# Optimization experiments

Measured on AMD Instinct MI355X. Metric: run time of the kernel, lower is better.

The kernel has to match this reference:

```python
import jax, jax.numpy as jnp
import numpy as np

N_NODES = 40000
N_EDGES = 640000
N_GRAPHS = 64
DIM_IN = 32
N_EDGE_TYPE = 16
DH = 128
DOUT = 256
T = 4


def setup_inputs() -> dict:
    key = jax.random.key(0)
    ks = jax.random.split(key, 16)
    inp = {
        "x": jax.random.normal(ks[0], (N_NODES, DIM_IN), dtype=jnp.float32),
        "edge_index": jax.random.randint(ks[1], (2, N_EDGES), 0, N_NODES, dtype=jnp.int64),
        "edge_attr": jax.random.normal(ks[2], (N_EDGES, N_EDGE_TYPE), dtype=jnp.float32),
        "graph_ids": jnp.sort(jax.random.randint(ks[3], (N_NODES,), 0, N_GRAPHS, dtype=jnp.int64)),
    }
    s = lambda fan_in: 1.0 / np.sqrt(fan_in)
    inp["Wn"] = jax.random.uniform(ks[4], (DIM_IN, DH), jnp.float32, -s(DIM_IN), s(DIM_IN))
    inp["bn"] = jnp.zeros((DH,), jnp.float32)
    inp["We"] = jax.random.uniform(ks[5], (N_EDGE_TYPE, DH), jnp.float32, -s(N_EDGE_TYPE), s(N_EDGE_TYPE))
    inp["be"] = jnp.zeros((DH,), jnp.float32)
    inp["W1"] = jax.random.uniform(ks[6], (DH, DH), jnp.float32, -s(DH), s(DH))
    inp["b1"] = jnp.zeros((DH,), jnp.float32)
    inp["W2"] = jax.random.uniform(ks[7], (DH, DH), jnp.float32, -s(DH), s(DH))
    inp["b2"] = jnp.zeros((DH,), jnp.float32)
    inp["Wl"] = jax.random.uniform(ks[8], (DH * T, DOUT), jnp.float32, -s(DH * T), s(DH * T))
    inp["bl"] = jnp.zeros((DOUT,), jnp.float32)
    return inp


def reference(x, edge_index, edge_attr, graph_ids, Wn, bn, We, be, W1, b1, W2, b2, Wl, bl):
    # node / edge input transforms
    h = x @ Wn + bn                      # [N, DH]
    e = edge_attr @ We + be              # [E, DH]
    src, dst = edge_index[0], edge_index[1]

    def mlp(z):
        return jax.nn.relu(z @ W1 + b1) @ W2 + b2

    all_h = []
    for _ in range(T):
        # GINE: message = relu(x_src + edge_attr), scatter-sum to dst
        msg = jax.nn.relu(h[src] + e)                                 # [E, DH]
        agg = jax.ops.segment_sum(msg, dst, num_segments=N_NODES)     # [N, DH]
        h = mlp(h + agg)                                              # eps = 0 -> (1+eps)*x = x
        all_h.append(h)

    all_x = jnp.concatenate(all_h, axis=-1)                           # [N, DH*T]
    pooled = jax.ops.segment_sum(all_x, graph_ids, num_segments=N_GRAPHS)  # [G, DH*T]
    return pooled @ Wl + bl                                           # [G, DOUT]
```

## Files before the change

kernel.cpp:

```cpp
#include <hip/hip_runtime.h>

#define N_NODES   40000
#define N_EDGES   640000
#define N_GRAPHS  64
#define DIM_IN    32
#define N_ETYPE   16
#define DH        128
#define DOUT      256
#define T_ITERS   4
#define SCAN_BLK  40

typedef unsigned int uint32;
typedef unsigned short ushort16;
typedef __attribute__((ext_vector_type(8))) short bf16x8;
typedef __attribute__((ext_vector_type(4))) float f32x4;

__device__ __forceinline__ uint32 f2bf1(float f) {
  uint32 u = __float_as_uint(f);
  return (u + 0x7fffu + ((u >> 16) & 1u)) >> 16;
}
__device__ __forceinline__ uint32 pack_bf2(float lo, float hi) {
  return (f2bf1(hi) << 16) | f2bf1(lo);
}

__global__ __launch_bounds__(256) void k_embed(const float* __restrict__ x,
                                               const float* __restrict__ Wn,
                                               const float* __restrict__ bn,
                                               float* __restrict__ h,
                                               ushort16* __restrict__ hb) {
  int idx = blockIdx.x * 256 + threadIdx.x;
  int n = idx >> 7, c = idx & 127;
  const float* xr = x + n * DIM_IN;
  float acc = bn[c];
#pragma unroll
  for (int k = 0; k < DIM_IN; ++k)
    acc = fmaf(xr[k], Wn[k * DH + c], acc);
  h[idx] = acc;
  hb[idx] = (ushort16)f2bf1(acc);
}

__global__ __launch_bounds__(256) void k_hist(const int* __restrict__ dst,
                                              int* __restrict__ counts) {
  int i = blockIdx.x * 256 + threadIdx.x;
  atomicAdd(&counts[dst[i]], 1);
}

__global__ __launch_bounds__(1024) void k_scan1(const int* __restrict__ counts,
                                                int* __restrict__ excl,
                                                int* __restrict__ blk_sums) {
  __shared__ int wsums[16];
  int tid = threadIdx.x, lane = tid & 63, w = tid >> 6;
  int i = blockIdx.x * 1024 + tid;
  int v = (i < N_NODES) ? counts[i] : 0;
  int s = v;
#pragma unroll
  for (int off = 1; off < 64; off <<= 1) {
    int t = __shfl_up(s, off);
    if (lane >= off) s += t;
  }
  if (lane == 63) wsums[w] = s;
  __syncthreads();
  if (tid < 16) {
    int ws_ = wsums[tid];
#pragma unroll
    for (int off = 1; off < 16; off <<= 1) {
      int t = __shfl_up(ws_, off);
      if (tid >= off) ws_ += t;
    }
    wsums[tid] = ws_;
  }
  __syncthreads();
  int e = s - v + (w ? wsums[w - 1] : 0);
  if (i < N_NODES) excl[i] = e;
  if (tid == 0) blk_sums[blockIdx.x] = wsums[15];
}

__global__ __launch_bounds__(64) void k_scan2(const int* __restrict__ blk_sums,
                                              int* __restrict__ blk_off,
                                              int* __restrict__ row_start) {
  int lane = threadIdx.x;
  int v = (lane < SCAN_BLK) ? blk_sums[lane] : 0;
  int s = v;
#pragma unroll
  for (int off = 1; off < 64; off <<= 1) {
    int t = __shfl_up(s, off);
    if (lane >= off) s += t;
  }
  if (lane < SCAN_BLK) blk_off[lane] = s - v;
  if (lane == 63) row_start[N_NODES] = s;
}

__global__ __launch_bounds__(1024) void k_scan3(int* __restrict__ row_start,
                                                const int* __restrict__ blk_off,
                                                int* __restrict__ cursor) {
  int i = blockIdx.x * 1024 + threadIdx.x;
  if (i < N_NODES) {
    int v = row_start[i] + blk_off[blockIdx.x];
    row_start[i] = v;
    cursor[i] = v;
  }
}

__global__ __launch_bounds__(256) void k_permute(const int* __restrict__ src,
                                                 const int* __restrict__ dst,
                                                 int* __restrict__ cursor,
                                                 int* __restrict__ src_perm,
                                                 int* __restrict__ eid_perm) {
  int i = blockIdx.x * 256 + threadIdx.x;
  int d = dst[i];
  int pos = atomicAdd(&cursor[d], 1);
  src_perm[pos] = src[i];
  eid_perm[pos] = i;
}

__global__ __launch_bounds__(256) void k_permute_ea(const int* __restrict__ src,
                                                    const int* __restrict__ dst,
                                                    const float4* __restrict__ edge_attr,
                                                    int* __restrict__ cursor,
                                                    int* __restrict__ src_perm,
                                                    float4* __restrict__ ea_perm) {
  int i = blockIdx.x * 256 + threadIdx.x;
  int d = dst[i];
  int pos = atomicAdd(&cursor[d], 1);
  src_perm[pos] = src[i];
  const float4* s = edge_attr + ((size_t)i << 2);
  float4* o = ea_perm + ((size_t)pos << 2);
  float4 v0 = s[0], v1 = s[1], v2 = s[2], v3 = s[3];
  o[0] = v0; o[1] = v1; o[2] = v2; o[3] = v3;
}

#define MAC16(A0,A1,A2,A3)                                          \
  p0 = fmaf(A0.x, we0[0], p0);  p1 = fmaf(A0.x, we1[0], p1);        \
  p0 = fmaf(A0.y, we0[1], p0);  p1 = fmaf(A0.y, we1[1], p1);        \
  p0 = fmaf(A0.z, we0[2], p0);  p1 = fmaf(A0.z, we1[2], p1);        \
  p0 = fmaf(A0.w, we0[3], p0);  p1 = fmaf(A0.w, we1[3], p1);        \
  p0 = fmaf(A1.x, we0[4], p0);  p1 = fmaf(A1.x, we1[4], p1);        \
  p0 = fmaf(A1.y, we0[5], p0);  p1 = fmaf(A1.y, we1[5], p1);        \
  p0 = fmaf(A1.z, we0[6], p0);  p1 = fmaf(A1.z, we1[6], p1);        \
  p0 = fmaf(A1.w, we0[7], p0);  p1 = fmaf(A1.w, we1[7], p1);        \
  p0 = fmaf(A2.x, we0[8], p0);  p1 = fmaf(A2.x, we1[8], p1);        \
  p0 = fmaf(A2.y, we0[9], p0);  p1 = fmaf(A2.y, we1[9], p1);        \
  p0 = fmaf(A2.z, we0[10], p0); p1 = fmaf(A2.z, we1[10], p1);       \
  p0 = fmaf(A2.w, we0[11], p0); p1 = fmaf(A2.w, we1[11], p1);       \
  p0 = fmaf(A3.x, we0[12], p0); p1 = fmaf(A3.x, we1[12], p1);       \
  p0 = fmaf(A3.y, we0[13], p0); p1 = fmaf(A3.y, we1[13], p1);       \
  p0 = fmaf(A3.z, we0[14], p0); p1 = fmaf(A3.z, we1[14], p1);       \
  p0 = fmaf(A3.w, we0[15], p0); p1 = fmaf(A3.w, we1[15], p1);

#define RELU_ACC(G)                                                  \
  acc0 += fmaxf(__uint_as_float((G) << 16) + p0, 0.0f);              \
  acc1 += fmaxf(__uint_as_float((G) & 0xffff0000u) + p1, 0.0f);

#define ACC2(G,E)                                                                 \
  acc0 += fmaxf(__uint_as_float((G) << 16) + __uint_as_float((E) << 16), 0.0f);   \
  acc1 += fmaxf(__uint_as_float((G) & 0xffff0000u) +                              \
                __uint_as_float((E) & 0xffff0000u), 0.0f);

__global__ __launch_bounds__(256) void k_perm_e(const int* __restrict__ src,
                                                const int* __restrict__ dst,
                                                const float4* __restrict__ edge_attr,
                                                const float* __restrict__ We,
                                                const float* __restrict__ be,
                                                int* __restrict__ cursor,
                                                int* __restrict__ src_perm,
                                                uint32* __restrict__ e_perm) {
  __shared__ float4 sAttr[1024];
  __shared__ int spos[256];
  int tid = threadIdx.x;
  int i = blockIdx.x * 256 + tid;
  int d = dst[i];
  int pos = atomicAdd(&cursor[d], 1);
  src_perm[pos] = src[i];
  spos[tid] = pos;
  size_t blockBase = (size_t)blockIdx.x * 1024;
  for (int idx = tid; idx < 1024; idx += 256)
    sAttr[idx] = edge_attr[blockBase + idx];
  __syncthreads();
  int lane = tid & 63, wv = tid >> 6;
  int c = lane << 1;
  float we0[N_ETYPE], we1[N_ETYPE];
#pragma unroll
  for (int k = 0; k < N_ETYPE; ++k) {
    we0[k] = We[k * DH + c];
    we1[k] = We[k * DH + c + 1];
  }
  float be0 = be[c], be1 = be[c + 1];
  const float4* a = &sAttr[wv << 8];
  const int* wp = &spos[wv << 6];
#pragma unroll 2
  for (int j = 0; j < 64; ++j) {
    int pos_j = wp[j];
    float4 a0 = a[j * 4 + 0], a1 = a[j * 4 + 1], a2 = a[j * 4 + 2], a3 = a[j * 4 + 3];
    float p0 = be0, p1 = be1;
    MAC16(a0, a1, a2, a3)
    e_perm[((size_t)pos_j << 6) + lane] = pack_bf2(p0, p1);
  }
}

__global__ __launch_bounds__(256) void k_agg_lite(const float* __restrict__ h,
                                                  const uint32* __restrict__ hb,
                                                  const uint32* __restrict__ e_perm,
                                                  const int* __restrict__ row_start,
                                                  const int* __restrict__ src_perm,
                                                  uint32* __restrict__ zb) {
  int lane = threadIdx.x & 63;
  int n = (blockIdx.x << 2) + (threadIdx.x >> 6);
  int c = lane << 1;
  float2 hself = *(const float2*)&h[(size_t)n * DH + c];
  float acc0 = hself.x, acc1 = hself.y;
  int beg = row_start[n], end = row_start[n + 1];
  const uint32* ep = e_perm + ((size_t)beg << 6) + lane;
  const int* sp = src_perm + beg;
  int m = end - beg;
  int i = 0;
  for (; i + 16 <= m; i += 16, ep += 1024, sp += 16) {
    int ss[16];
    uint32 gg[16], ee[16];
#pragma unroll
    for (int k = 0; k < 16; ++k) ss[k] = sp[k];
#pragma unroll
    for (int k = 0; k < 16; ++k) gg[k] = hb[((size_t)ss[k] << 6) + lane];
#pragma unroll
    for (int k = 0; k < 16; ++k) ee[k] = ep[k * 64];
#pragma unroll
    for (int k = 0; k < 16; ++k) { ACC2(gg[k], ee[k]) }
  }
  for (; i + 4 <= m; i += 4, ep += 256, sp += 4) {
    int ss[4];
    uint32 gg[4], ee[4];
#pragma unroll
    for (int k = 0; k < 4; ++k) ss[k] = sp[k];
#pragma unroll
    for (int k = 0; k < 4; ++k) gg[k] = hb[((size_t)ss[k] << 6) + lane];
#pragma unroll
    for (int k = 0; k < 4; ++k) ee[k] = ep[k * 64];
#pragma unroll
    for (int k = 0; k < 4; ++k) { ACC2(gg[k], ee[k]) }
  }
  for (; i < m; ++i, ep += 64, ++sp) {
    int s0 = sp[0];
    uint32 g0 = hb[((size_t)s0 << 6) + lane];
    uint32 e0 = ep[0];
    ACC2(g0, e0)
  }
  zb[(size_t)n * 64 + lane] = pack_bf2(acc0, acc1);
}

__global__ __launch_bounds__(256) void k_agg_seq(const float* __restrict__ h,
                                                 const uint32* __restrict__ hb,
                                                 const float4* __restrict__ ea_perm,
                                                 const float* __restrict__ We,
                                                 const float* __restrict__ be,
                                                 const int* __restrict__ row_start,
                                                 const int* __restrict__ src_perm,
                                                 float* __restrict__ z) {
  int lane = threadIdx.x & 63;
  int n = (blockIdx.x << 2) + (threadIdx.x >> 6);
  int c = lane << 1;
  float we0[N_ETYPE], we1[N_ETYPE];
#pragma unroll
  for (int k = 0; k < N_ETYPE; ++k) {
    we0[k] = We[k * DH + c];
    we1[k] = We[k * DH + c + 1];
  }
  float be0 = be[c], be1 = be[c + 1];
  float2 hself = *(const float2*)&h[(size_t)n * DH + c];
  float acc0 = hself.x, acc1 = hself.y;
  int beg = row_start[n], end = row_start[n + 1];
  const float4* ea = ea_perm + ((size_t)beg << 2);
  int i = beg;
  for (; i + 4 <= end; i += 4, ea += 16) {
    int s0 = src_perm[i], s1 = src_perm[i + 1], s2 = src_perm[i + 2], s3 = src_perm[i + 3];
    uint32 g0 = hb[((size_t)s0 << 6) + lane];
    uint32 g1 = hb[((size_t)s1 << 6) + lane];
    uint32 g2 = hb[((size_t)s2 << 6) + lane];
    uint32 g3 = hb[((size_t)s3 << 6) + lane];
    float4 a0 = ea[0], a1 = ea[1], a2 = ea[2], a3 = ea[3];
    float4 b0 = ea[4], b1v = ea[5], b2v = ea[6], b3 = ea[7];
    float p0, p1;
    p0 = be0; p1 = be1; MAC16(a0, a1, a2, a3) RELU_ACC(g0)
    p0 = be0; p1 = be1; MAC16(b0, b1v, b2v, b3) RELU_ACC(g1)
    a0 = ea[8]; a1 = ea[9]; a2 = ea[10]; a3 = ea[11];
    b0 = ea[12]; b1v = ea[13]; b2v = ea[14]; b3 = ea[15];
    p0 = be0; p1 = be1; MAC16(a0, a1, a2, a3) RELU_ACC(g2)
    p0 = be0; p1 = be1; MAC16(b0, b1v, b2v, b3) RELU_ACC(g3)
  }
  for (; i < end; ++i, ea += 4) {
    int s0 = src_perm[i];
    uint32 g0 = hb[((size_t)s0 << 6) + lane];
    float4 a0 = ea[0], a1 = ea[1], a2 = ea[2], a3 = ea[3];
    float p0 = be0, p1 = be1;
    MAC16(a0, a1, a2, a3) RELU_ACC(g0)
  }
  *(float2*)&z[(size_t)n * DH + c] = make_float2(acc0, acc1);
}

__global__ __launch_bounds__(256, 8) void k_agg_ind(const float* __restrict__ h,
                                                    const uint32* __restrict__ hb,
                                                    const float* __restrict__ edge_attr,
                                                    const float* __restrict__ We,
                                                    const float* __restrict__ be,
                                                    const int* __restrict__ row_start,
                                                    const int* __restrict__ src_perm,
                                                    const int* __restrict__ eid_perm,
                                                    float* __restrict__ z) {
  int lane = threadIdx.x & 63;
  int n = (blockIdx.x << 2) + (threadIdx.x >> 6);
  int c = lane << 1;
  float we0[N_ETYPE], we1[N_ETYPE];
#pragma unroll
  for (int k = 0; k < N_ETYPE; ++k) {
    we0[k] = We[k * DH + c];
    we1[k] = We[k * DH + c + 1];
  }
  float be0 = be[c], be1 = be[c + 1];
  float2 hself = *(const float2*)&h[(size_t)n * DH + c];
  float acc0 = hself.x, acc1 = hself.y;
  int beg = row_start[n], end = row_start[n + 1];
  int i = beg;
  for (; i + 1 < end; i += 2) {
    int s0 = src_perm[i], s1 = src_perm[i + 1];
    int e0i = eid_perm[i], e1i = eid_perm[i + 1];
    uint32 g0 = hb[((size_t)s0 << 6) + lane];
    uint32 g1 = hb[((size_t)s1 << 6) + lane];
    const float4* eA = (const float4*)(edge_attr + (size_t)e0i * N_ETYPE);
    const float4* eB = (const float4*)(edge_attr + (size_t)e1i * N_ETYPE);
    float4 a0 = eA[0], a1 = eA[1], a2 = eA[2], a3 = eA[3];
    float p0, p1;
    p0 = be0; p1 = be1; MAC16(a0, a1, a2, a3) RELU_ACC(g0)
    float4 b0 = eB[0], b1v = eB[1], b2v = eB[2], b3 = eB[3];
    p0 = be0; p1 = be1; MAC16(b0, b1v, b2v, b3) RELU_ACC(g1)
  }
  if (i < end) {
    int s0 = src_perm[i];
    int e0i = eid_perm[i];
    uint32 g0 = hb[((size_t)s0 << 6) + lane];
    const float4* eA = (const float4*)(edge_attr + (size_t)e0i * N_ETYPE);
    float4 a0 = eA[0], a1 = eA[1], a2 = eA[2], a3 = eA[3];
    float p0 = be0, p1 = be1;
    MAC16(a0, a1, a2, a3) RELU_ACC(g0)
  }
  *(float2*)&z[(size_t)n * DH + c] = make_float2(acc0, acc1);
}

__global__ __launch_bounds__(256) void k_prep_w(const float* __restrict__ W1,
                                                const float* __restrict__ W2,
                                                ushort16* __restrict__ w1t,
                                                ushort16* __restrict__ w2t) {
  int id = blockIdx.x * 256 + threadIdx.x;
  int which = id >> 14;
  int rem = id & 16383;
  int k = rem >> 7, n = rem & 127;
  const float* W = which ? W2 : W1;
  ushort16* wt = which ? w2t : w1t;
  wt[n * 128 + k] = (ushort16)f2bf1(W[k * 128 + n]);
}

__global__ __launch_bounds__(256) void k_mlp_mfma(const uint32* __restrict__ zb,
                                                  const ushort16* __restrict__ w1t,
                                                  const ushort16* __restrict__ w2t,
                                                  const float* __restrict__ b1,
                                                  const float* __restrict__ b2,
                                                  const int* __restrict__ graph_ids,
                                                  float* __restrict__ h_out,
                                                  ushort16* __restrict__ hb_out,
                                                  float* __restrict__ pooled,
                                                  int t_slot) {
  __shared__ ushort16 sW[128 * 136];
  __shared__ ushort16 sA[64 * 136];
  int tid = threadIdx.x;
  int rb = blockIdx.x * 64;

  for (int idx = tid; idx < 1024; idx += 256) {
    int row = idx >> 4, ch = idx & 15;
    *(uint4*)&sA[row * 136 + ch * 8] = *(const uint4*)&zb[(size_t)(rb + row) * 64 + ch * 4];
  }
  for (int idx = tid; idx < 2048; idx += 256) {
    int row = idx >> 4, ch = idx & 15;
    *(uint4*)&sW[row * 136 + ch * 8] = *(const uint4*)&w1t[row * 128 + ch * 8];
  }
  __syncthreads();

  int l = tid & 63, w = tid >> 6;
  int r = l & 15, g = l >> 4;

  f32x4 acc[8];
#pragma unroll
  for (int n = 0; n < 8; ++n) {
    float bv = b1[n * 16 + r];
    acc[n] = (f32x4){bv, bv, bv, bv};
  }
#pragma unroll
  for (int k0 = 0; k0 < 4; ++k0) {
    bf16x8 a = *(const bf16x8*)&sA[(w * 16 + r) * 136 + k0 * 32 + g * 8];
#pragma unroll
    for (int n = 0; n < 8; ++n) {
      bf16x8 b = *(const bf16x8*)&sW[(n * 16 + r) * 136 + k0 * 32 + g * 8];
      acc[n] = __builtin_amdgcn_mfma_f32_16x16x32_bf16(a, b, acc[n], 0, 0, 0);
    }
  }
#pragma unroll
  for (int n = 0; n < 8; ++n) {
#pragma unroll
    for (int q = 0; q < 4; ++q) {
      float v = fmaxf(acc[n][q], 0.0f);
      sA[(w * 16 + g * 4 + q) * 136 + n * 16 + r] = (ushort16)f2bf1(v);
    }
  }
  __syncthreads();
  for (int idx = tid; idx < 2048; idx += 256) {
    int row = idx >> 4, ch = idx & 15;
    *(uint4*)&sW[row * 136 + ch * 8] = *(const uint4*)&w2t[row * 128 + ch * 8];
  }
  __syncthreads();

#pragma unroll
  for (int n = 0; n < 8; ++n) {
    float bv = b2[n * 16 + r];
    acc[n] = (f32x4){bv, bv, bv, bv};
  }
#pragma unroll
  for (int k0 = 0; k0 < 4; ++k0) {
    bf16x8 a = *(const bf16x8*)&sA[(w * 16 + r) * 136 + k0 * 32 + g * 8];
#pragma unroll
    for (int n = 0; n < 8; ++n) {
      bf16x8 b = *(const bf16x8*)&sW[(n * 16 + r) * 136 + k0 * 32 + g * 8];
      acc[n] = __builtin_amdgcn_mfma_f32_16x16x32_bf16(a, b, acc[n], 0, 0, 0);
    }
  }

  int node0 = rb + w * 16;
#pragma unroll
  for (int n = 0; n < 8; ++n) {
#pragma unroll
    for (int q = 0; q < 4; ++q) {
      int node = node0 + g * 4 + q;
      float v = acc[n][q];
      h_out[(size_t)node * DH + n * 16 + r] = v;
      hb_out[(size_t)node * DH + n * 16 + r] = (ushort16)f2bf1(v);
    }
  }
  float* pbase = pooled + t_slot * DH;
  int gid0 = graph_ids[node0];
  if (gid0 == graph_ids[node0 + 15]) {
#pragma unroll
    for (int n = 0; n < 8; ++n) {
      float s = acc[n][0] + acc[n][1] + acc[n][2] + acc[n][3];
      s += __shfl_xor(s, 16);
      s += __shfl_xor(s, 32);
      if (l < 16) atomicAdd(&pbase[gid0 * 512 + n * 16 + r], s);
    }
  } else {
#pragma unroll
    for (int q = 0; q < 4; ++q) {
      int node = node0 + g * 4 + q;
      int gg = graph_ids[node];
#pragma unroll
      for (int n = 0; n < 8; ++n)
        atomicAdd(&pbase[gg * 512 + n * 16 + r], acc[n][q]);
    }
  }
}

#define MLPFMA(K, U0, U1)                                            \
  {                                                                  \
    _Pragma("unroll")                                                \
    for (int i_ = 0; i_ < 8; ++i_) {                                 \
      float2 a_ = *(const float2*)&sA[(r0 + i_) * 132 + (K)];        \
      acc[i_][0] = fmaf(a_.x, U0.x, acc[i_][0]);                     \
      acc[i_][1] = fmaf(a_.x, U0.y, acc[i_][1]);                     \
      acc[i_][2] = fmaf(a_.x, U0.z, acc[i_][2]);                     \
      acc[i_][3] = fmaf(a_.x, U0.w, acc[i_][3]);                     \
      acc[i_][0] = fmaf(a_.y, U1.x, acc[i_][0]);                     \
      acc[i_][1] = fmaf(a_.y, U1.y, acc[i_][1]);                     \
      acc[i_][2] = fmaf(a_.y, U1.z, acc[i_][2]);                     \
      acc[i_][3] = fmaf(a_.y, U1.w, acc[i_][3]);                     \
    }                                                                \
  }

__device__ __forceinline__ void gemm_tile_g(const float* sA, const float4* __restrict__ Wv,
                                            float acc[8][4], int r0, int cg) {
  float4 c0 = Wv[cg],       c1 = Wv[32 + cg];
  float4 n0 = Wv[64 + cg],  n1 = Wv[96 + cg];
#pragma unroll 4
  for (int k = 0; k < DH - 4; k += 2) {
    float4 u0 = c0, u1 = c1;
    c0 = n0; c1 = n1;
    n0 = Wv[(k + 4) * 32 + cg];
    n1 = Wv[(k + 5) * 32 + cg];
    MLPFMA(k, u0, u1)
  }
  MLPFMA(DH - 4, c0, c1)
  MLPFMA(DH - 2, n0, n1)
}

__global__ __launch_bounds__(256) void k_mlp(const float* __restrict__ z,
                                             const float* __restrict__ W1,
                                             const float* __restrict__ b1,
                                             const float* __restrict__ W2,
                                             const float* __restrict__ b2,
                                             const int* __restrict__ graph_ids,
                                             float* __restrict__ h_out,
                                             uint32* __restrict__ hb_out,
                                             float* __restrict__ pooled,
                                             int t_slot) {
  __shared__ float sA[64 * 132];
  int tid = threadIdx.x;
  int rb = blockIdx.x * 64;
  for (int idx = tid; idx < 64 * 32; idx += 256) {
    int r = idx >> 5, kq = (idx & 31) << 2;
    *(float4*)&sA[r * 132 + kq] = *(const float4*)&z[(size_t)(rb + r) * DH + kq];
  }
  __syncthreads();

  int cg = tid & 31, rg = tid >> 5;
  int c0 = cg << 2, r0 = rg << 3;
  float acc[8][4];
  {
    float4 bb = *(const float4*)&b1[c0];
#pragma unroll
    for (int i = 0; i < 8; ++i) { acc[i][0] = bb.x; acc[i][1] = bb.y; acc[i][2] = bb.z; acc[i][3] = bb.w; }
  }
  gemm_tile_g(sA, (const float4*)W1, acc, r0, cg);
  __syncthreads();
#pragma unroll
  for (int i = 0; i < 8; ++i) {
    float4 v;
    v.x = fmaxf(acc[i][0], 0.0f); v.y = fmaxf(acc[i][1], 0.0f);
    v.z = fmaxf(acc[i][2], 0.0f); v.w = fmaxf(acc[i][3], 0.0f);
    *(float4*)&sA[(r0 + i) * 132 + c0] = v;
  }
  __syncthreads();
  {
    float4 bb = *(const float4*)&b2[c0];
#pragma unroll
    for (int i = 0; i < 8; ++i) { acc[i][0] = bb.x; acc[i][1] = bb.y; acc[i][2] = bb.z; acc[i][3] = bb.w; }
  }
  gemm_tile_g(sA, (const float4*)W2, acc, r0, cg);

  int node0 = rb + r0;
#pragma unroll
  for (int i = 0; i < 8; ++i) {
    float4 v = make_float4(acc[i][0], acc[i][1], acc[i][2], acc[i][3]);
    *(float4*)&h_out[(size_t)(node0 + i) * DH + c0] = v;
    uint2 hv;
    hv.x = pack_bf2(acc[i][0], acc[i][1]);
    hv.y = pack_bf2(acc[i][2], acc[i][3]);
    *(uint2*)&hb_out[(size_t)(node0 + i) * 64 + (c0 >> 1)] = hv;
  }
  float* pbase = pooled + t_slot * DH;
  int g_first = graph_ids[node0];
  int g_last = graph_ids[node0 + 7];
  if (g_first == g_last) {
    float s0 = 0.f, s1 = 0.f, s2 = 0.f, s3 = 0.f;
#pragma unroll
    for (int i = 0; i < 8; ++i) { s0 += acc[i][0]; s1 += acc[i][1]; s2 += acc[i][2]; s3 += acc[i][3]; }
    atomicAdd(&pbase[g_first * 512 + c0 + 0], s0);
    atomicAdd(&pbase[g_first * 512 + c0 + 1], s1);
    atomicAdd(&pbase[g_first * 512 + c0 + 2], s2);
    atomicAdd(&pbase[g_first * 512 + c0 + 3], s3);
  } else {
#pragma unroll
    for (int i = 0; i < 8; ++i) {
      int g = graph_ids[node0 + i];
      atomicAdd(&pbase[g * 512 + c0 + 0], acc[i][0]);
      atomicAdd(&pbase[g * 512 + c0 + 1], acc[i][1]);
      atomicAdd(&pbase[g * 512 + c0 + 2], acc[i][2]);
      atomicAdd(&pbase[g * 512 + c0 + 3], acc[i][3]);
    }
  }
}

__global__ __launch_bounds__(256) void k_final(const float* __restrict__ pooled,
                                               const float* __restrict__ Wl,
                                               const float* __restrict__ bl,
                                               float* __restrict__ out) {
  int g = blockIdx.x, o = threadIdx.x;
  __shared__ float sp[DH * T_ITERS];
  for (int idx = o; idx < DH * T_ITERS; idx += 256) sp[idx] = pooled[g * (DH * T_ITERS) + idx];
  __syncthreads();
  float acc = bl[o];
#pragma unroll 8
  for (int j = 0; j < DH * T_ITERS; ++j)
    acc = fmaf(sp[j], Wl[j * DOUT + o], acc);
  out[g * DOUT + o] = acc;
}

extern "C" void kernel_launch(void* const* d_in, const int* in_sizes, int n_in,
                              void* d_out, int out_size, void* d_ws, size_t ws_size,
                              hipStream_t stream) {
  const float* x         = (const float*)d_in[0];
  const int*   edge_index= (const int*)d_in[1];
  const float* edge_attr = (const float*)d_in[2];
  const int*   graph_ids = (const int*)d_in[3];
  const float* Wn = (const float*)d_in[4];
  const float* bn = (const float*)d_in[5];
  const float* We = (const float*)d_in[6];
  const float* be = (const float*)d_in[7];
  const float* W1 = (const float*)d_in[8];
  const float* b1 = (const float*)d_in[9];
  const float* W2 = (const float*)d_in[10];
  const float* b2 = (const float*)d_in[11];
  const float* Wl = (const float*)d_in[12];
  const float* bl = (const float*)d_in[13];
  float* out = (float*)d_out;

  char* p = (char*)d_ws;
  auto alloc = [&](size_t bytes) { char* r = p; p += (bytes + 255) & ~(size_t)255; return r; };
  float*  h        = (float*)alloc((size_t)N_NODES * DH * 4);
  float*  z        = (float*)alloc((size_t)N_NODES * DH * 4);
  uint32* hb       = (uint32*)alloc((size_t)N_NODES * DH * 2);
  float*  pooled   = (float*)alloc((size_t)N_GRAPHS * DH * T_ITERS * 4);
  int*    counts   = (int*)alloc((size_t)N_NODES * 4);
  int*    row_start= (int*)alloc((size_t)(N_NODES + 1) * 4);
  int*    cursor   = (int*)alloc((size_t)N_NODES * 4);
  int*    src_perm = (int*)alloc((size_t)N_EDGES * 4);
  int*    blk_sums = (int*)alloc(256);
  int*    blk_off  = (int*)alloc(256);

  const int* src = edge_index;
  const int* dst = edge_index + N_EDGES;

  size_t used = (size_t)(p - (char*)d_ws);
  size_t need_e  = used + (size_t)N_EDGES * DH * 2 + 4096;
  size_t need_ea = used + (size_t)N_EDGES * N_ETYPE * 4 + 4096;

  hipMemsetAsync(counts, 0, (size_t)N_NODES * 4, stream);
  hipMemsetAsync(pooled, 0, (size_t)N_GRAPHS * DH * T_ITERS * 4, stream);

  k_embed<<<N_NODES * DH / 256, 256, 0, stream>>>(x, Wn, bn, h, (ushort16*)hb);
  k_hist<<<N_EDGES / 256, 256, 0, stream>>>(dst, counts);
  k_scan1<<<SCAN_BLK, 1024, 0, stream>>>(counts, row_start, blk_sums);
  k_scan2<<<1, 64, 0, stream>>>(blk_sums, blk_off, row_start);
  k_scan3<<<SCAN_BLK, 1024, 0, stream>>>(row_start, blk_off, cursor);

  if (ws_size >= need_e) {
    uint32* e_perm = (uint32*)alloc((size_t)N_EDGES * DH * 2);
    uint32* zb = (uint32*)z;
    ushort16* w1t = (ushort16*)counts;
    ushort16* w2t = w1t + 128 * 128;
    k_prep_w<<<128, 256, 0, stream>>>(W1, W2, w1t, w2t);
    k_perm_e<<<N_EDGES / 256, 256, 0, stream>>>(src, dst, (const float4*)edge_attr,
                                                We, be, cursor, src_perm, e_perm);
    for (int t = 0; t < T_ITERS; ++t) {
      k_agg_lite<<<N_NODES / 4, 256, 0, stream>>>(h, hb, e_perm, row_start, src_perm, zb);
      k_mlp_mfma<<<N_NODES / 64, 256, 0, stream>>>(zb, w1t, w2t, b1, b2, graph_ids,
                                                   h, (ushort16*)hb, pooled, t);
    }
  } else if (ws_size >= need_ea) {
    float4* ea_perm = (float4*)alloc((size_t)N_EDGES * N_ETYPE * 4);
    k_permute_ea<<<N_EDGES / 256, 256, 0, stream>>>(src, dst, (const float4*)edge_attr,
                                                    cursor, src_perm, ea_perm);
    for (int t = 0; t < T_ITERS; ++t) {
      k_agg_seq<<<N_NODES / 4, 256, 0, stream>>>(h, hb, ea_perm, We, be, row_start, src_perm, z);
      k_mlp<<<N_NODES / 64, 256, 0, stream>>>(z, W1, b1, W2, b2, graph_ids, h, hb, pooled, t);
    }
  } else {
    int* eid_perm = (int*)alloc((size_t)N_EDGES * 4);
    k_permute<<<N_EDGES / 256, 256, 0, stream>>>(src, dst, cursor, src_perm, eid_perm);
    for (int t = 0; t < T_ITERS; ++t) {
      k_agg_ind<<<N_NODES / 4, 256, 0, stream>>>(h, hb, edge_attr, We, be, row_start, src_perm, eid_perm, z);
      k_mlp<<<N_NODES / 64, 256, 0, stream>>>(z, W1, b1, W2, b2, graph_ids, h, hb, pooled, t);
    }
  }
  k_final<<<N_GRAPHS, 256, 0, stream>>>(pooled, Wl, bl, out);
}
```

Measured before the change: 466.6 us.

## Drop fp32 h buffer, stream MLP weights from registers, coalesce bf16 stores

The aggregation kernel now reads the self term from the bf16 hidden buffer, and the MLP kernel no longer writes the fp32 hidden state. MLP weight fragments are loaded directly from global memory into registers with one-step prefetch, instead of being staged in shared memory. This shrinks LDS usage and removes barriers. Output bf16 rows are staged through shared memory for coalesced stores. The self term now loses precision by being rounded to bf16.

```diff
diff --git a/kernel.cpp b/kernel.cpp
--- a/kernel.cpp
+++ b/kernel.cpp
@@ -197,17 +197,16 @@
   }
 }
 
-__global__ __launch_bounds__(256) void k_agg_lite(const float* __restrict__ h,
-                                                  const uint32* __restrict__ hb,
+__global__ __launch_bounds__(256) void k_agg_lite(const uint32* __restrict__ hb,
                                                   const uint32* __restrict__ e_perm,
                                                   const int* __restrict__ row_start,
                                                   const int* __restrict__ src_perm,
                                                   uint32* __restrict__ zb) {
   int lane = threadIdx.x & 63;
   int n = (blockIdx.x << 2) + (threadIdx.x >> 6);
-  int c = lane << 1;
-  float2 hself = *(const float2*)&h[(size_t)n * DH + c];
-  float acc0 = hself.x, acc1 = hself.y;
+  uint32 hself = hb[(size_t)n * 64 + lane];
+  float acc0 = __uint_as_float(hself << 16);
+  float acc1 = __uint_as_float(hself & 0xffff0000u);
   int beg = row_start[n], end = row_start[n + 1];
   const uint32* ep = e_perm + ((size_t)beg << 6) + lane;
   const int* sp = src_perm + beg;
@@ -362,11 +361,9 @@
                                                   const float* __restrict__ b1,
                                                   const float* __restrict__ b2,
                                                   const int* __restrict__ graph_ids,
-                                                  float* __restrict__ h_out,
-                                                  ushort16* __restrict__ hb_out,
+                                                  uint32* __restrict__ hb_out,
                                                   float* __restrict__ pooled,
                                                   int t_slot) {
-  __shared__ ushort16 sW[128 * 136];
   __shared__ ushort16 sA[64 * 136];
   int tid = threadIdx.x;
   int rb = blockIdx.x * 64;
@@ -375,14 +372,16 @@
     int row = idx >> 4, ch = idx & 15;
     *(uint4*)&sA[row * 136 + ch * 8] = *(const uint4*)&zb[(size_t)(rb + row) * 64 + ch * 4];
   }
-  for (int idx = tid; idx < 2048; idx += 256) {
-    int row = idx >> 4, ch = idx & 15;
-    *(uint4*)&sW[row * 136 + ch * 8] = *(const uint4*)&w1t[row * 128 + ch * 8];
-  }
-  __syncthreads();
 
   int l = tid & 63, w = tid >> 6;
   int r = l & 15, g = l >> 4;
+  const ushort16* w1p = w1t + r * 128 + g * 8;
+  const ushort16* w2p = w2t + r * 128 + g * 8;
+
+  bf16x8 bf[8];
+#pragma unroll
+  for (int n = 0; n < 8; ++n)
+    bf[n] = *(const bf16x8*)(w1p + n * 2048);
 
   f32x4 acc[8];
 #pragma unroll
@@ -390,57 +389,55 @@
     float bv = b1[n * 16 + r];
     acc[n] = (f32x4){bv, bv, bv, bv};
   }
+  __syncthreads();
+
+  const ushort16* aBase = &sA[(w * 16 + r) * 136 + g * 8];
+
 #pragma unroll
   for (int k0 = 0; k0 < 4; ++k0) {
-    bf16x8 a = *(const bf16x8*)&sA[(w * 16 + r) * 136 + k0 * 32 + g * 8];
-#pragma unroll
-    for (int n = 0; n < 8; ++n) {
-      bf16x8 b = *(const bf16x8*)&sW[(n * 16 + r) * 136 + k0 * 32 + g * 8];
-      acc[n] = __builtin_amdgcn_mfma_f32_16x16x32_bf16(a, b, acc[n], 0, 0, 0);
-    }
-  }
-#pragma unroll
-  for (int n = 0; n < 8; ++n) {
-#pragma unroll
-    for (int q = 0; q < 4; ++q) {
-      float v = fmaxf(acc[n][q], 0.0f);
-      sA[(w * 16 + g * 4 + q) * 136 + n * 16 + r] = (ushort16)f2bf1(v);
-    }
-  }
-  __syncthreads();
-  for (int idx = tid; idx < 2048; idx += 256) {
-    int row = idx >> 4, ch = idx & 15;
-    *(uint4*)&sW[row * 136 + ch * 8] = *(const uint4*)&w2t[row * 128 + ch * 8];
-  }
-  __syncthreads();
+    bf16x8 a = *(const bf16x8*)(aBase + k0 * 32);
+    bf16x8 cur[8];
+#pragma unroll
+    for (int n = 0; n < 8; ++n) cur[n] = bf[n];
+#pragma unroll
+    for (int n = 0; n < 8; ++n)
+      bf[n] = (k0 < 3) ? *(const bf16x8*)(w1p + n * 2048 + (k0 + 1) * 32)
+                       : *(const bf16x8*)(w2p + n * 2048);
+#pragma unroll
+    for (int n = 0; n < 8; ++n)
+      acc[n] = __builtin_amdgcn_mfma_f32_16x16x32_bf16(a, cur[n], acc[n], 0, 0, 0);
+  }
+
+#pragma unroll
+  for (int n = 0; n < 8; ++n)
+#pragma unroll
+    for (int q = 0; q < 4; ++q)
+      sA[(w * 16 + g * 4 + q) * 136 + n * 16 + r] = (ushort16)f2bf1(fmaxf(acc[n][q], 0.0f));
 
 #pragma unroll
   for (int n = 0; n < 8; ++n) {
     float bv = b2[n * 16 + r];
     acc[n] = (f32x4){bv, bv, bv, bv};
   }
+
 #pragma unroll
   for (int k0 = 0; k0 < 4; ++k0) {
-    bf16x8 a = *(const bf16x8*)&sA[(w * 16 + r) * 136 + k0 * 32 + g * 8];
-#pragma unroll
-    for (int n = 0; n < 8; ++n) {
-      bf16x8 b = *(const bf16x8*)&sW[(n * 16 + r) * 136 + k0 * 32 + g * 8];
-      acc[n] = __builtin_amdgcn_mfma_f32_16x16x32_bf16(a, b, acc[n], 0, 0, 0);
-    }
-  }
-
+    bf16x8 a = *(const bf16x8*)(aBase + k0 * 32);
+    bf16x8 cur[8];
+#pragma unroll
+    for (int n = 0; n < 8; ++n) cur[n] = bf[n];
+    if (k0 < 3) {
+#pragma unroll
+      for (int n = 0; n < 8; ++n)
+        bf[n] = *(const bf16x8*)(w2p + n * 2048 + (k0 + 1) * 32);
+    }
+#pragma unroll
+    for (int n = 0; n < 8; ++n)
+      acc[n] = __builtin_amdgcn_mfma_f32_16x16x32_bf16(a, cur[n], acc[n], 0, 0, 0);
+  }
+
+  float* pbase = pooled + t_slot * DH;
   int node0 = rb + w * 16;
-#pragma unroll
-  for (int n = 0; n < 8; ++n) {
-#pragma unroll
-    for (int q = 0; q < 4; ++q) {
-      int node = node0 + g * 4 + q;
-      float v = acc[n][q];
-      h_out[(size_t)node * DH + n * 16 + r] = v;
-      hb_out[(size_t)node * DH + n * 16 + r] = (ushort16)f2bf1(v);
-    }
-  }
-  float* pbase = pooled + t_slot * DH;
   int gid0 = graph_ids[node0];
   if (gid0 == graph_ids[node0 + 15]) {
 #pragma unroll
@@ -459,6 +456,18 @@
       for (int n = 0; n < 8; ++n)
         atomicAdd(&pbase[gg * 512 + n * 16 + r], acc[n][q]);
     }
+  }
+
+#pragma unroll
+  for (int n = 0; n < 8; ++n)
+#pragma unroll
+    for (int q = 0; q < 4; ++q)
+      sA[(w * 16 + g * 4 + q) * 136 + n * 16 + r] = (ushort16)f2bf1(acc[n][q]);
+  __syncthreads();
+  for (int idx = tid; idx < 4096; idx += 256) {
+    int row = idx >> 6, dw = idx & 63;
+    uint32 v = *(const uint32*)&sA[row * 136 + dw * 2];
+    hb_out[(size_t)(rb + row) * 64 + dw] = v;
   }
 }
 
@@ -643,9 +652,9 @@
     k_perm_e<<<N_EDGES / 256, 256, 0, stream>>>(src, dst, (const float4*)edge_attr,
                                                 We, be, cursor, src_perm, e_perm);
     for (int t = 0; t < T_ITERS; ++t) {
-      k_agg_lite<<<N_NODES / 4, 256, 0, stream>>>(h, hb, e_perm, row_start, src_perm, zb);
+      k_agg_lite<<<N_NODES / 4, 256, 0, stream>>>(hb, e_perm, row_start, src_perm, zb);
       k_mlp_mfma<<<N_NODES / 64, 256, 0, stream>>>(zb, w1t, w2t, b1, b2, graph_ids,
-                                                   h, (ushort16*)hb, pooled, t);
+                                                   hb, pooled, t);
     }
   } else if (ws_size >= need_ea) {
     float4* ea_perm = (float4*)alloc((size_t)N_EDGES * N_ETYPE * 4);
```

Measured after the change: 488.8 us. 1.05x slower.
